# Performance work log

Hardware: AMD Instinct MI355X
Metric: run time of the kernel (lower is better)

Reference implementation:

```python
import jax, jax.numpy as jnp
import numpy as np
import math

B, H, S, D = 2, 8, 2048, 64

def setup_inputs() -> dict:
    key = jax.random.key(0)
    kq, kk, kv = jax.random.split(key, 3)
    q = jax.random.normal(kq, (B, H, S, D), dtype=jnp.float32)
    k = jax.random.normal(kk, (B, H, S, D), dtype=jnp.float32)
    v = jax.random.normal(kv, (B, H, S, D), dtype=jnp.float32)
    # causal mask: True means masked (filled with -1e9), matching masked_fill
    mask = jnp.triu(jnp.ones((S, S), dtype=jnp.bool_), k=1)
    return {"q": q, "k": k, "v": v, "mask": mask}

def reference(q, k, v, mask) -> jnp.ndarray:
    d_model = q.shape[-1]
    # [..., s, t] scores
    att = jnp.einsum('bhsd,bhtd->bhst', q, k) / math.sqrt(d_model)
    if mask is not None:
        # broadcast mask over leading dims; True -> -1e9
        att = jnp.where(mask, jnp.float32(-1e9), att)
    # numerically stable softmax over last axis (matches manual Softmax)
    att = jax.nn.softmax(att, axis=-1)
    return jnp.einsum('bhst,bhtd->bhsd', att, v)
```

## Files before the change

kernel.cpp:

```cpp
#include <hip/hip_runtime.h>

typedef __bf16 bf16x8 __attribute__((ext_vector_type(8)));
typedef float  f32x16 __attribute__((ext_vector_type(16)));

constexpr int Sn  = 2048;
constexpr int Dh  = 64;
constexpr int QT  = 32;
constexpr int KVT = 32;
constexpr int NBH = 16;
constexpr int NT  = Sn / QT;
constexpr int NW  = 8;
constexpr int TSTR = 4 * 64 * 8;

constexpr float SCL = 0.125f * 1.44269504088896340736f;

constexpr size_t ELEMS  = (size_t)NBH * Sn * Dh;
constexpr size_t QB_OFF = 0;
constexpr size_t KP_OFF = ELEMS;
constexpr size_t VP_OFF = 2 * ELEMS;
constexpr size_t WS_NEED = 3 * ELEMS * 2;

__device__ inline bf16x8 cvt8(float4 a, float4 b, float s) {
  bf16x8 r;
  r[0] = (__bf16)(a.x * s); r[1] = (__bf16)(a.y * s);
  r[2] = (__bf16)(a.z * s); r[3] = (__bf16)(a.w * s);
  r[4] = (__bf16)(b.x * s); r[5] = (__bf16)(b.y * s);
  r[6] = (__bf16)(b.z * s); r[7] = (__bf16)(b.w * s);
  return r;
}

__global__ __launch_bounds__(256) void prep(
    const float* __restrict__ q, const float* __restrict__ k,
    const float* __restrict__ v, __bf16* __restrict__ ws)
{
  __shared__ float tl[KVT][Dh + 1];
  const int g    = blockIdx.x;
  const int tid  = threadIdx.x;
  const int wv   = tid >> 6;
  const int lane = tid & 63;
  const int hi   = lane >> 5;
  const int ln   = lane & 31;
  const size_t tbase = (size_t)g * (KVT * Dh);

  {
    const float* qp = q + tbase + (size_t)tid * 8;
    const float4 a = *(const float4*)qp;
    const float4 b = *(const float4*)(qp + 4);
    *(bf16x8*)(ws + QB_OFF + tbase + (size_t)tid * 8) = cvt8(a, b, SCL);
  }
  {
    const float* kp = k + tbase;
#pragma unroll
    for (int e = 0; e < 2; ++e) {
      const int i4  = tid + e * 256;
      const float4 x = *(const float4*)(kp + (size_t)i4 * 4);
      const int row = i4 >> 4, col = (i4 & 15) * 4;
      tl[row][col] = x.x; tl[row][col + 1] = x.y;
      tl[row][col + 2] = x.z; tl[row][col + 3] = x.w;
    }
  }
  __syncthreads();
  {
    bf16x8 r;
#pragma unroll
    for (int i = 0; i < 8; ++i) r[i] = (__bf16)tl[ln][16 * wv + 8 * hi + i];
    *(bf16x8*)(ws + KP_OFF + ((size_t)(g * 4 + wv) * 64 + lane) * 8) = r;
  }
  __syncthreads();
  {
    const float* vp = v + tbase;
#pragma unroll
    for (int e = 0; e < 2; ++e) {
      const int i4  = tid + e * 256;
      const float4 x = *(const float4*)(vp + (size_t)i4 * 4);
      const int row = i4 >> 4, col = (i4 & 15) * 4;
      tl[row][col] = x.x; tl[row][col + 1] = x.y;
      tl[row][col + 2] = x.z; tl[row][col + 3] = x.w;
    }
  }
  __syncthreads();
  {
    const int dt = wv >> 1, T = wv & 1;
    bf16x8 r;
#pragma unroll
    for (int i = 0; i < 8; ++i) {
      const int row = 16 * T + 4 * hi + (i & 3) + 8 * (i >> 2);
      r[i] = (__bf16)tl[row][32 * dt + ln];
    }
    *(bf16x8*)(ws + VP_OFF + ((size_t)(g * 4 + wv) * 64 + lane) * 8) = r;
  }
}

#define LOADKV(K0,K1,K2,K3,V0,V1,V2,V3,kt_) do {                         \
    const __bf16* kp_ = kpB + (size_t)(kt_) * TSTR + lane * 8;           \
    K0 = *(const bf16x8*)(kp_);                                          \
    K1 = *(const bf16x8*)(kp_ + 512);                                    \
    K2 = *(const bf16x8*)(kp_ + 1024);                                   \
    K3 = *(const bf16x8*)(kp_ + 1536);                                   \
    const __bf16* vp_ = vpB + (size_t)(kt_) * TSTR + lane * 8;           \
    V0 = *(const bf16x8*)(vp_);                                          \
    V1 = *(const bf16x8*)(vp_ + 512);                                    \
    V2 = *(const bf16x8*)(vp_ + 1024);                                   \
    V3 = *(const bf16x8*)(vp_ + 1536);                                   \
  } while (0)

#define COMPUTE(K0,K1,K2,K3,V0,V1,V2,V3,kt_) do {                        \
    f32x16 st;                                                           \
    _Pragma("unroll")                                                    \
    for (int i_ = 0; i_ < 16; ++i_) st[i_] = 0.f;                        \
    __builtin_amdgcn_s_setprio(1);                                       \
    st = __builtin_amdgcn_mfma_f32_32x32x16_bf16(K0, qf[0], st, 0, 0, 0);\
    st = __builtin_amdgcn_mfma_f32_32x32x16_bf16(K1, qf[1], st, 0, 0, 0);\
    st = __builtin_amdgcn_mfma_f32_32x32x16_bf16(K2, qf[2], st, 0, 0, 0);\
    st = __builtin_amdgcn_mfma_f32_32x32x16_bf16(K3, qf[3], st, 0, 0, 0);\
    __builtin_amdgcn_s_setprio(0);                                       \
    if ((kt_) == tile) {                                                 \
      _Pragma("unroll")                                                  \
      for (int r_ = 0; r_ < 16; ++r_) {                                  \
        const int tl_ = (r_ & 3) + 8 * (r_ >> 2) + 4 * hi;               \
        if (tl_ > ln) st[r_] = -1e30f;                                   \
      }                                                                  \
    }                                                                    \
    float p[16];                                                         \
    _Pragma("unroll")                                                    \
    for (int r_ = 0; r_ < 16; ++r_) p[r_] = __builtin_amdgcn_exp2f(st[r_]); \
    bf16x8 pa0, pa1;                                                     \
    _Pragma("unroll")                                                    \
    for (int i_ = 0; i_ < 8; ++i_) { pa0[i_] = (__bf16)p[i_]; pa1[i_] = (__bf16)p[8 + i_]; } \
    __builtin_amdgcn_s_setprio(1);                                       \
    o0 = __builtin_amdgcn_mfma_f32_32x32x16_bf16(pa0, V0, o0, 0, 0, 0);  \
    o1 = __builtin_amdgcn_mfma_f32_32x32x16_bf16(pa0, V2, o1, 0, 0, 0);  \
    ls = __builtin_amdgcn_mfma_f32_32x32x16_bf16(pa0, ONESV, ls, 0, 0, 0);\
    o0 = __builtin_amdgcn_mfma_f32_32x32x16_bf16(pa1, V1, o0, 0, 0, 0);  \
    o1 = __builtin_amdgcn_mfma_f32_32x32x16_bf16(pa1, V3, o1, 0, 0, 0);  \
    ls = __builtin_amdgcn_mfma_f32_32x32x16_bf16(pa1, ONESV, ls, 0, 0, 0);\
    __builtin_amdgcn_s_setprio(0);                                       \
  } while (0)

__global__ __launch_bounds__(512) void attn_bf16(
    const __bf16* __restrict__ ws, float* __restrict__ og)
{
  __shared__ __bf16 ldsO[NW][QT][Dh];
  __shared__ float  ldsL[NW][QT];

  const int b    = blockIdx.x;
  const int bh   = b & 15;
  const int pr   = b >> 4;
  const int tid  = threadIdx.x;
  const int w    = tid >> 6;
  const int lane = tid & 63;
  const int hi   = lane >> 5;
  const int ln   = lane & 31;

  const __bf16* qB  = ws + QB_OFF + (size_t)bh * Sn * Dh;
  const __bf16* kpB = ws + KP_OFF + (size_t)bh * NT * TSTR;
  const __bf16* vpB = ws + VP_OFF + (size_t)bh * NT * TSTR;

  bf16x8 ONESV;
#pragma unroll
  for (int i = 0; i < 8; ++i) ONESV[i] = (__bf16)1.0f;

  for (int ph = 0; ph < 2; ++ph) {
    const int tile = ph ? (63 - pr) : pr;

    bf16x8 qf[4];
    {
      const __bf16* qp = qB + ((size_t)(tile * QT + ln)) * Dh + 8 * hi;
#pragma unroll
      for (int c = 0; c < 4; ++c) qf[c] = *(const bf16x8*)(qp + 16 * c);
    }

    f32x16 o0, o1, ls;
#pragma unroll
    for (int i = 0; i < 16; ++i) { o0[i] = 0.f; o1[i] = 0.f; ls[i] = 0.f; }

    bf16x8 kA0, kA1, kA2, kA3, vA0, vA1, vA2, vA3;
    bf16x8 kB0, kB1, kB2, kB3, vB0, vB1, vB2, vB3;

    int kt = w;
    bool tailA = true;
    if (kt <= tile) LOADKV(kA0,kA1,kA2,kA3,vA0,vA1,vA2,vA3, kt);
    while (kt + NW <= tile) {
      LOADKV(kB0,kB1,kB2,kB3,vB0,vB1,vB2,vB3, kt + NW);
      COMPUTE(kA0,kA1,kA2,kA3,vA0,vA1,vA2,vA3, kt);
      kt += NW;
      if (kt + NW <= tile) {
        LOADKV(kA0,kA1,kA2,kA3,vA0,vA1,vA2,vA3, kt + NW);
        COMPUTE(kB0,kB1,kB2,kB3,vB0,vB1,vB2,vB3, kt);
        kt += NW;
      } else {
        COMPUTE(kB0,kB1,kB2,kB3,vB0,vB1,vB2,vB3, kt);
        kt += NW;
        tailA = false;
      }
    }
    if (tailA && kt <= tile) COMPUTE(kA0,kA1,kA2,kA3,vA0,vA1,vA2,vA3, kt);

#pragma unroll
    for (int r = 0; r < 16; ++r) {
      const int rl = (r & 3) + 8 * (r >> 2) + 4 * hi;
      ldsO[w][rl][ln]      = (__bf16)o0[r];
      ldsO[w][rl][32 + ln] = (__bf16)o1[r];
      if (ln == 0) ldsL[w][rl] = ls[r];
    }
    __syncthreads();

#pragma unroll
    for (int e = 0; e < 4; ++e) {
      const int i   = e * 512 + tid;
      const int row = i >> 6;
      const int col = i & 63;
      float L = 0.f, o = 0.f;
#pragma unroll
      for (int wv = 0; wv < NW; ++wv) {
        L += ldsL[wv][row];
        o += (float)ldsO[wv][row][col];
      }
      og[((size_t)bh * Sn + tile * QT + row) * Dh + col] = o / L;
    }
    __syncthreads();
  }
}

__global__ __launch_bounds__(256) void attn_f32(
    const float* __restrict__ qg, const float* __restrict__ kg,
    const float* __restrict__ vg, float* __restrict__ og)
{
  __shared__ float ldsO[4][QT][Dh];
  __shared__ float ldsM[4][QT];
  __shared__ float ldsL[4][QT];

  const int g    = blockIdx.x;
  const int bh   = g >> 6;
  const int idx  = g & 63;
  const int tile = (idx & 1) ? (63 - (idx >> 1)) : (idx >> 1);
  const int w    = threadIdx.x >> 6;
  const int lane = threadIdx.x & 63;
  const int hi   = lane >> 5;
  const int ln   = lane & 31;

  const size_t base = (size_t)bh * Sn * Dh;
  const float* Q = qg + base;
  const float* K = kg + base;
  const float* V = vg + base;
  float*       O = og + base;
  const int srow = tile * QT + ln;

  bf16x8 qf[4];
  {
    const float* qp = Q + (size_t)srow * Dh + 8 * hi;
#pragma unroll
    for (int c = 0; c < 4; ++c) {
      const float4 x = *(const float4*)(qp + 16 * c);
      const float4 y = *(const float4*)(qp + 16 * c + 4);
      qf[c] = cvt8(x, y, 0.125f);
    }
  }
  f32x16 o0, o1;
#pragma unroll
  for (int i = 0; i < 16; ++i) { o0[i] = 0.f; o1[i] = 0.f; }
  float m = -1e30f, lsum = 0.f;

  for (int kt = w; kt <= tile; kt += 4) {
    const int t0 = kt * KVT;
    bf16x8 kf[4];
    const float* kp = K + (size_t)(t0 + ln) * Dh + 8 * hi;
#pragma unroll
    for (int c = 0; c < 4; ++c) {
      const float4 x = *(const float4*)(kp + 16 * c);
      const float4 y = *(const float4*)(kp + 16 * c + 4);
      kf[c] = cvt8(x, y, 1.0f);
    }
    f32x16 st;
#pragma unroll
    for (int i = 0; i < 16; ++i) st[i] = 0.f;
#pragma unroll
    for (int c = 0; c < 4; ++c)
      st = __builtin_amdgcn_mfma_f32_32x32x16_bf16(kf[c], qf[c], st, 0, 0, 0);
    if (kt == tile) {
#pragma unroll
      for (int r = 0; r < 16; ++r) {
        const int tl = (r & 3) + 8 * (r >> 2) + 4 * hi;
        if (tl > ln) st[r] = -1e30f;
      }
    }
    float tmax = st[0];
#pragma unroll
    for (int r = 1; r < 16; ++r) tmax = fmaxf(tmax, st[r]);
    tmax = fmaxf(tmax, __shfl_xor(tmax, 32));
    const float mnew = fmaxf(m, tmax);
    const bool  resc = __any(mnew > m);
    const float corr = __expf(m - mnew);
    m = mnew;
    float p[16];
    float psum = 0.f;
#pragma unroll
    for (int r = 0; r < 16; ++r) { p[r] = __expf(st[r] - mnew); psum += p[r]; }
    psum += __shfl_xor(psum, 32);
    lsum = lsum * corr + psum;
    if (resc) {
#pragma unroll
      for (int r = 0; r < 16; ++r) {
        const float cr = __shfl(corr, (r & 3) + 8 * (r >> 2) + 4 * hi);
        o0[r] *= cr; o1[r] *= cr;
      }
    }
    bf16x8 pa0, pa1;
#pragma unroll
    for (int i = 0; i < 8; ++i) { pa0[i] = (__bf16)p[i]; pa1[i] = (__bf16)p[8 + i]; }
#pragma unroll
    for (int T = 0; T < 2; ++T) {
      const int tb = t0 + 16 * T + 4 * hi;
      bf16x8 vb0, vb1;
#pragma unroll
      for (int j = 0; j < 4; ++j) {
        const float* vp  = V + (size_t)(tb + j) * Dh + ln;
        const float* vp2 = V + (size_t)(tb + 8 + j) * Dh + ln;
        vb0[j]     = (__bf16)vp[0];
        vb1[j]     = (__bf16)vp[32];
        vb0[4 + j] = (__bf16)vp2[0];
        vb1[4 + j] = (__bf16)vp2[32];
      }
      const bf16x8 pa = T ? pa1 : pa0;
      o0 = __builtin_amdgcn_mfma_f32_32x32x16_bf16(pa, vb0, o0, 0, 0, 0);
      o1 = __builtin_amdgcn_mfma_f32_32x32x16_bf16(pa, vb1, o1, 0, 0, 0);
    }
  }
#pragma unroll
  for (int r = 0; r < 16; ++r) {
    const int rl = (r & 3) + 8 * (r >> 2) + 4 * hi;
    ldsO[w][rl][ln]      = o0[r];
    ldsO[w][rl][32 + ln] = o1[r];
  }
  if (hi == 0) { ldsM[w][ln] = m; ldsL[w][ln] = lsum; }
  __syncthreads();
  const int tid = threadIdx.x;
#pragma unroll
  for (int e = 0; e < 8; ++e) {
    const int i   = e * 256 + tid;
    const int row = i >> 6;
    const int col = i & 63;
    const float m0 = ldsM[0][row], m1 = ldsM[1][row], m2 = ldsM[2][row], m3 = ldsM[3][row];
    const float M  = fmaxf(fmaxf(m0, m1), fmaxf(m2, m3));
    const float e0 = __expf(m0 - M), e1 = __expf(m1 - M), e2 = __expf(m2 - M), e3 = __expf(m3 - M);
    const float L  = ldsL[0][row] * e0 + ldsL[1][row] * e1 + ldsL[2][row] * e2 + ldsL[3][row] * e3;
    const float o  = ldsO[0][row][col] * e0 + ldsO[1][row][col] * e1
                   + ldsO[2][row][col] * e2 + ldsO[3][row][col] * e3;
    O[(size_t)(tile * QT + row) * Dh + col] = o / L;
  }
}

extern "C" void kernel_launch(void* const* d_in, const int* in_sizes, int n_in,
                              void* d_out, int out_size, void* d_ws, size_t ws_size,
                              hipStream_t stream) {
  const float* q = (const float*)d_in[0];
  const float* k = (const float*)d_in[1];
  const float* v = (const float*)d_in[2];
  float* out = (float*)d_out;
  if (ws_size >= WS_NEED) {
    prep<<<dim3(NBH * NT), dim3(256), 0, stream>>>(q, k, v, (__bf16*)d_ws);
    attn_bf16<<<dim3(NBH * NT / 2), dim3(512), 0, stream>>>((const __bf16*)d_ws, out);
  } else {
    attn_f32<<<dim3(1024), dim3(256), 0, stream>>>(q, k, v, out);
  }
}
```

Measured before the change: 36.17 us.

## One query tile per 4-wave block, heaviest first, separate masked diagonal step

```diff
diff --git a/kernel.cpp b/kernel.cpp
--- a/kernel.cpp
+++ b/kernel.cpp
@@ -9,7 +9,7 @@
 constexpr int KVT = 32;
 constexpr int NBH = 16;
 constexpr int NT  = Sn / QT;
-constexpr int NW  = 8;
+constexpr int NW  = 4;
 constexpr int TSTR = 4 * 64 * 8;
 
 constexpr float SCL = 0.125f * 1.44269504088896340736f;
@@ -104,48 +104,64 @@
     V3 = *(const bf16x8*)(vp_ + 1536);                                   \
   } while (0)
 
-#define COMPUTE(K0,K1,K2,K3,V0,V1,V2,V3,kt_) do {                        \
+#define COMPUTE_NM(K0,K1,K2,K3,V0,V1,V2,V3) do {                         \
     f32x16 st;                                                           \
     _Pragma("unroll")                                                    \
     for (int i_ = 0; i_ < 16; ++i_) st[i_] = 0.f;                        \
-    __builtin_amdgcn_s_setprio(1);                                       \
     st = __builtin_amdgcn_mfma_f32_32x32x16_bf16(K0, qf[0], st, 0, 0, 0);\
     st = __builtin_amdgcn_mfma_f32_32x32x16_bf16(K1, qf[1], st, 0, 0, 0);\
     st = __builtin_amdgcn_mfma_f32_32x32x16_bf16(K2, qf[2], st, 0, 0, 0);\
     st = __builtin_amdgcn_mfma_f32_32x32x16_bf16(K3, qf[3], st, 0, 0, 0);\
-    __builtin_amdgcn_s_setprio(0);                                       \
-    if ((kt_) == tile) {                                                 \
-      _Pragma("unroll")                                                  \
-      for (int r_ = 0; r_ < 16; ++r_) {                                  \
-        const int tl_ = (r_ & 3) + 8 * (r_ >> 2) + 4 * hi;               \
-        if (tl_ > ln) st[r_] = -1e30f;                                   \
-      }                                                                  \
-    }                                                                    \
     float p[16];                                                         \
     _Pragma("unroll")                                                    \
     for (int r_ = 0; r_ < 16; ++r_) p[r_] = __builtin_amdgcn_exp2f(st[r_]); \
     bf16x8 pa0, pa1;                                                     \
     _Pragma("unroll")                                                    \
     for (int i_ = 0; i_ < 8; ++i_) { pa0[i_] = (__bf16)p[i_]; pa1[i_] = (__bf16)p[8 + i_]; } \
-    __builtin_amdgcn_s_setprio(1);                                       \
     o0 = __builtin_amdgcn_mfma_f32_32x32x16_bf16(pa0, V0, o0, 0, 0, 0);  \
     o1 = __builtin_amdgcn_mfma_f32_32x32x16_bf16(pa0, V2, o1, 0, 0, 0);  \
     ls = __builtin_amdgcn_mfma_f32_32x32x16_bf16(pa0, ONESV, ls, 0, 0, 0);\
     o0 = __builtin_amdgcn_mfma_f32_32x32x16_bf16(pa1, V1, o0, 0, 0, 0);  \
     o1 = __builtin_amdgcn_mfma_f32_32x32x16_bf16(pa1, V3, o1, 0, 0, 0);  \
     ls = __builtin_amdgcn_mfma_f32_32x32x16_bf16(pa1, ONESV, ls, 0, 0, 0);\
-    __builtin_amdgcn_s_setprio(0);                                       \
   } while (0)
 
-__global__ __launch_bounds__(512) void attn_bf16(
+#define COMPUTE_MS(K0,K1,K2,K3,V0,V1,V2,V3) do {                         \
+    f32x16 st;                                                           \
+    _Pragma("unroll")                                                    \
+    for (int i_ = 0; i_ < 16; ++i_) st[i_] = 0.f;                        \
+    st = __builtin_amdgcn_mfma_f32_32x32x16_bf16(K0, qf[0], st, 0, 0, 0);\
+    st = __builtin_amdgcn_mfma_f32_32x32x16_bf16(K1, qf[1], st, 0, 0, 0);\
+    st = __builtin_amdgcn_mfma_f32_32x32x16_bf16(K2, qf[2], st, 0, 0, 0);\
+    st = __builtin_amdgcn_mfma_f32_32x32x16_bf16(K3, qf[3], st, 0, 0, 0);\
+    _Pragma("unroll")                                                    \
+    for (int r_ = 0; r_ < 16; ++r_) {                                    \
+      const int tl_ = (r_ & 3) + 8 * (r_ >> 2) + 4 * hi;                 \
+      if (tl_ > ln) st[r_] = -1e30f;                                     \
+    }                                                                    \
+    float p[16];                                                         \
+    _Pragma("unroll")                                                    \
+    for (int r_ = 0; r_ < 16; ++r_) p[r_] = __builtin_amdgcn_exp2f(st[r_]); \
+    bf16x8 pa0, pa1;                                                     \
+    _Pragma("unroll")                                                    \
+    for (int i_ = 0; i_ < 8; ++i_) { pa0[i_] = (__bf16)p[i_]; pa1[i_] = (__bf16)p[8 + i_]; } \
+    o0 = __builtin_amdgcn_mfma_f32_32x32x16_bf16(pa0, V0, o0, 0, 0, 0);  \
+    o1 = __builtin_amdgcn_mfma_f32_32x32x16_bf16(pa0, V2, o1, 0, 0, 0);  \
+    ls = __builtin_amdgcn_mfma_f32_32x32x16_bf16(pa0, ONESV, ls, 0, 0, 0);\
+    o0 = __builtin_amdgcn_mfma_f32_32x32x16_bf16(pa1, V1, o0, 0, 0, 0);  \
+    o1 = __builtin_amdgcn_mfma_f32_32x32x16_bf16(pa1, V3, o1, 0, 0, 0);  \
+    ls = __builtin_amdgcn_mfma_f32_32x32x16_bf16(pa1, ONESV, ls, 0, 0, 0);\
+  } while (0)
+
+__global__ __launch_bounds__(256) void attn_bf16(
     const __bf16* __restrict__ ws, float* __restrict__ og)
 {
   __shared__ __bf16 ldsO[NW][QT][Dh];
   __shared__ float  ldsL[NW][QT];
 
   const int b    = blockIdx.x;
-  const int bh   = b & 15;
-  const int pr   = b >> 4;
+  const int bh   = 2 * (b & 7) + ((b >> 3) & 1);
+  const int tile = 63 - (b >> 4);
   const int tid  = threadIdx.x;
   const int w    = tid >> 6;
   const int lane = tid & 63;
@@ -160,65 +176,59 @@
 #pragma unroll
   for (int i = 0; i < 8; ++i) ONESV[i] = (__bf16)1.0f;
 
-  for (int ph = 0; ph < 2; ++ph) {
-    const int tile = ph ? (63 - pr) : pr;
-
-    bf16x8 qf[4];
-    {
-      const __bf16* qp = qB + ((size_t)(tile * QT + ln)) * Dh + 8 * hi;
-#pragma unroll
-      for (int c = 0; c < 4; ++c) qf[c] = *(const bf16x8*)(qp + 16 * c);
-    }
-
-    f32x16 o0, o1, ls;
-#pragma unroll
-    for (int i = 0; i < 16; ++i) { o0[i] = 0.f; o1[i] = 0.f; ls[i] = 0.f; }
-
-    bf16x8 kA0, kA1, kA2, kA3, vA0, vA1, vA2, vA3;
-    bf16x8 kB0, kB1, kB2, kB3, vB0, vB1, vB2, vB3;
-
-    int kt = w;
-    bool tailA = true;
-    if (kt <= tile) LOADKV(kA0,kA1,kA2,kA3,vA0,vA1,vA2,vA3, kt);
-    while (kt + NW <= tile) {
-      LOADKV(kB0,kB1,kB2,kB3,vB0,vB1,vB2,vB3, kt + NW);
-      COMPUTE(kA0,kA1,kA2,kA3,vA0,vA1,vA2,vA3, kt);
-      kt += NW;
-      if (kt + NW <= tile) {
-        LOADKV(kA0,kA1,kA2,kA3,vA0,vA1,vA2,vA3, kt + NW);
-        COMPUTE(kB0,kB1,kB2,kB3,vB0,vB1,vB2,vB3, kt);
-        kt += NW;
-      } else {
-        COMPUTE(kB0,kB1,kB2,kB3,vB0,vB1,vB2,vB3, kt);
-        kt += NW;
-        tailA = false;
-      }
-    }
-    if (tailA && kt <= tile) COMPUTE(kA0,kA1,kA2,kA3,vA0,vA1,vA2,vA3, kt);
-
-#pragma unroll
-    for (int r = 0; r < 16; ++r) {
-      const int rl = (r & 3) + 8 * (r >> 2) + 4 * hi;
-      ldsO[w][rl][ln]      = (__bf16)o0[r];
-      ldsO[w][rl][32 + ln] = (__bf16)o1[r];
-      if (ln == 0) ldsL[w][rl] = ls[r];
-    }
-    __syncthreads();
-
-#pragma unroll
-    for (int e = 0; e < 4; ++e) {
-      const int i   = e * 512 + tid;
-      const int row = i >> 6;
-      const int col = i & 63;
-      float L = 0.f, o = 0.f;
-#pragma unroll
-      for (int wv = 0; wv < NW; ++wv) {
-        L += ldsL[wv][row];
-        o += (float)ldsO[wv][row][col];
-      }
-      og[((size_t)bh * Sn + tile * QT + row) * Dh + col] = o / L;
-    }
-    __syncthreads();
+  bf16x8 qf[4];
+  {
+    const __bf16* qp = qB + ((size_t)(tile * QT + ln)) * Dh + 8 * hi;
+#pragma unroll
+    for (int c = 0; c < 4; ++c) qf[c] = *(const bf16x8*)(qp + 16 * c);
+  }
+
+  f32x16 o0, o1, ls;
+#pragma unroll
+  for (int i = 0; i < 16; ++i) { o0[i] = 0.f; o1[i] = 0.f; ls[i] = 0.f; }
+
+  bf16x8 kA0, kA1, kA2, kA3, vA0, vA1, vA2, vA3;
+  bf16x8 kB0, kB1, kB2, kB3, vB0, vB1, vB2, vB3;
+
+  int kt = w;
+  while (kt + NW < tile) {
+    LOADKV(kA0,kA1,kA2,kA3,vA0,vA1,vA2,vA3, kt);
+    LOADKV(kB0,kB1,kB2,kB3,vB0,vB1,vB2,vB3, kt + NW);
+    COMPUTE_NM(kA0,kA1,kA2,kA3,vA0,vA1,vA2,vA3);
+    COMPUTE_NM(kB0,kB1,kB2,kB3,vB0,vB1,vB2,vB3);
+    kt += 2 * NW;
+  }
+  if (kt < tile) {
+    LOADKV(kA0,kA1,kA2,kA3,vA0,vA1,vA2,vA3, kt);
+    COMPUTE_NM(kA0,kA1,kA2,kA3,vA0,vA1,vA2,vA3);
+    kt += NW;
+  }
+  if (kt == tile) {
+    LOADKV(kA0,kA1,kA2,kA3,vA0,vA1,vA2,vA3, tile);
+    COMPUTE_MS(kA0,kA1,kA2,kA3,vA0,vA1,vA2,vA3);
+  }
+
+#pragma unroll
+  for (int r = 0; r < 16; ++r) {
+    const int rl = (r & 3) + 8 * (r >> 2) + 4 * hi;
+    ldsO[w][rl][ln]      = (__bf16)o0[r];
+    ldsO[w][rl][32 + ln] = (__bf16)o1[r];
+    if (ln == 0) ldsL[w][rl] = ls[r];
+  }
+  __syncthreads();
+
+#pragma unroll
+  for (int e = 0; e < 8; ++e) {
+    const int i   = e * 256 + tid;
+    const int row = i >> 6;
+    const int col = i & 63;
+    float L = 0.f, o = 0.f;
+#pragma unroll
+    for (int wv = 0; wv < NW; ++wv) {
+      L += ldsL[wv][row];
+      o += (float)ldsO[wv][row][col];
+    }
+    og[((size_t)bh * Sn + tile * QT + row) * Dh + col] = o / L;
   }
 }
 
@@ -359,7 +369,7 @@
   float* out = (float*)d_out;
   if (ws_size >= WS_NEED) {
     prep<<<dim3(NBH * NT), dim3(256), 0, stream>>>(q, k, v, (__bf16*)d_ws);
-    attn_bf16<<<dim3(NBH * NT / 2), dim3(512), 0, stream>>>((const __bf16*)d_ws, out);
+    attn_bf16<<<dim3(NBH * NT), dim3(256), 0, stream>>>((const __bf16*)d_ws, out);
   } else {
     attn_f32<<<dim3(1024), dim3(256), 0, stream>>>(q, k, v, out);
   }
```

Result: faster. 31.96 us (-11.6%).
